# Kernel tuning notes

Measured on AMD Instinct MI355X. Metric: run time of the kernel, lower is better.

Reference implementation:

```python
import jax, jax.numpy as jnp
import numpy as np

B, S = 2, 2048                 # batch, prefill seq len
H, HKV, D = 32, 8, 128          # num_heads, num_kv_heads, head_size
G = H // HKV                    # queries per kv head (GQA)
BLOCK_SIZE, NUM_BLOCKS = 128, 128
SCALE = 1.0 / (D ** 0.5)
NEG_INF = -1e9


def setup_inputs() -> dict:
    key = jax.random.key(0)
    kq, kk, kv, kc = jax.random.split(key, 4)
    query = jax.random.normal(kq, (B, S, H * D), dtype=jnp.float32)
    key_t = jax.random.normal(kk, (B, S, HKV * D), dtype=jnp.float32)
    value = jax.random.normal(kv, (B, S, HKV * D), dtype=jnp.float32)
    kv_cache = jax.random.normal(kc, (2, NUM_BLOCKS, BLOCK_SIZE, HKV, D), dtype=jnp.float32)
    tok = jnp.arange(B * S)
    block_indices = (tok // BLOCK_SIZE).astype(jnp.int32)   # in [0, NUM_BLOCKS)
    block_offsets = (tok % BLOCK_SIZE).astype(jnp.int32)    # in [0, BLOCK_SIZE)
    causal = jnp.tril(jnp.ones((S, S), dtype=bool))
    attn_bias = jnp.where(causal, 0.0, NEG_INF).astype(jnp.float32)[None, None]  # [1,1,S,S]
    return {"query": query, "key": key_t, "value": value, "kv_cache": kv_cache,
            "block_indices": block_indices, "block_offsets": block_offsets,
            "attn_bias": attn_bias}


def reference(query, key, value, kv_cache, block_indices, block_offsets, attn_bias):
    # --- KV cache scatter write (VLLMKVCache insert) ---
    k_tok = key.reshape(-1, HKV, D)     # [num_tokens, HKV, D]
    v_tok = value.reshape(-1, HKV, D)
    key_cache = kv_cache[0].at[block_indices, block_offsets].set(k_tok)
    value_cache = kv_cache[1].at[block_indices, block_offsets].set(v_tok)

    # --- prefill attention (xops.prompt_attention with GQA) ---
    q = query.reshape(B, S, HKV, G, D)            # split heads into kv groups
    kh = key.reshape(B, S, HKV, D)
    vh = value.reshape(B, S, HKV, D)
    scores = jnp.einsum('bqhgd,bkhd->bhgqk', q, kh) * SCALE  # [B,HKV,G,S,S]
    scores = scores + attn_bias[:, :, None]                   # bias broadcast over h,g
    probs = jax.nn.softmax(scores, axis=-1)
    out = jnp.einsum('bhgqk,bkhd->bqhgd', probs, vh)          # [B,S,HKV,G,D]
    output = out.reshape(B, S, H * D)
    return output, key_cache, value_cache
```

## Files before the change

kernel.cpp:

```cpp
#include <hip/hip_runtime.h>
#include <hip/hip_bf16.h>
#include <stdint.h>

#define B_ 2
#define S_ 2048
#define HKV_ 8
#define D_ 128

#define KVB 32
#define KTILE_SH 4096
#define VTILE_SH 4096
#define LDSBUF 16384
#define NCOPY 512
#define PLANE4 4194304
#define NSLOT 16384

typedef __attribute__((ext_vector_type(8))) short bf16x8;
typedef __attribute__((ext_vector_type(16))) float f32x16;
typedef __attribute__((ext_vector_type(4))) int int4v;

typedef const __attribute__((address_space(1))) void gv_t;
typedef __attribute__((address_space(3))) void lv_t;

__device__ __forceinline__ unsigned pk2(float lo, float hi) {
  unsigned r;
  asm("v_cvt_pk_bf16_f32 %0, %1, %2" : "=v"(r) : "v"(lo), "v"(hi));
  return r;
}
__device__ __forceinline__ void plswap(unsigned& a, unsigned& b) {
  asm volatile("v_permlane32_swap_b32 %0, %1" : "+v"(a), "+v"(b));
}
__device__ __forceinline__ bf16x8 frag4(unsigned a, unsigned b, unsigned c, unsigned d) {
  union { int4v i; bf16x8 v; } u;
  u.i = int4v{(int)a, (int)b, (int)c, (int)d};
  return u.v;
}


__global__ __launch_bounds__(256)
void prep_kernel(const float* __restrict__ K, const float* __restrict__ V,
                 const int* __restrict__ bi, const int* __restrict__ bo,
                 float* __restrict__ kc, float* __restrict__ vc,
                 short* __restrict__ kimg, short* __restrict__ vimg,
                 unsigned char* __restrict__ map) {
  __shared__ float Vf[KVB * 132];
  const int bid = blockIdx.x;
  const int hg  = bid & 15;
  const int kt  = bid >> 4;
  const int kvh = hg & 7;
  const int b   = hg >> 3;
  const int tid = threadIdx.x;
  const int kv0 = kt * KVB;
  const float* kb = K + (int64_t)b * S_ * 1024 + kvh * 128;
  const float* vb = V + (int64_t)b * S_ * 1024 + kvh * 128;
  short* kimg_t = kimg + (int64_t)(hg * 64 + kt) * KTILE_SH;
  short* vimg_t = vimg + (int64_t)(hg * 64 + kt) * VTILE_SH;
#pragma unroll
  for (int i = 0; i < 4; ++i) {
    int idx = i * 256 + tid;
    int key = idx >> 5;
    int d0  = (idx & 31) * 4;
    int64_t roff = (int64_t)(kv0 + key) * 1024 + d0;
    float4 kf = *(const float4*)(kb + roff);
    float4 vf = *(const float4*)(vb + roff);
    int tok = b * S_ + kv0 + key;
    int slot = bi[tok] * 128 + bo[tok];
    *(float4*)(kc + (int64_t)slot * 1024 + kvh * 128 + d0) = kf;
    *(float4*)(vc + (int64_t)slot * 1024 + kvh * 128 + d0) = vf;
    if (d0 == 0 && kvh == 0) map[slot] = 1;
    unsigned k01 = pk2(kf.x, kf.y), k23 = pk2(kf.z, kf.w);
    int koff = (d0 >> 3) * 256 + key * 8 + (d0 & 7);
    int2 st; st.x = (int)k01; st.y = (int)k23;
    *(int2*)(kimg_t + koff) = st;
    *(float4*)(&Vf[key * 132 + d0]) = vf;
  }
  __syncthreads();
  const int d  = tid & 127;
  const int kg = tid >> 7;
  const int k0 = kg * 16;
  unsigned uu[8];
#pragma unroll
  for (int i2 = 0; i2 < 8; ++i2)
    uu[i2] = pk2(Vf[(k0 + 2 * i2) * 132 + d], Vf[(k0 + 2 * i2 + 1) * 132 + d]);
  int vbase = ((d >> 5) * 4 + (k0 >> 4) * 2) * 256 + (d & 31) * 8;
  *(int4v*)(vimg_t + vbase)       = int4v{(int)uu[0], (int)uu[1], (int)uu[2], (int)uu[3]};
  *(int4v*)(vimg_t + vbase + 256) = int4v{(int)uu[4], (int)uu[5], (int)uu[6], (int)uu[7]};
}


__global__ __launch_bounds__(256, 4)
void fused_kernel(const float* __restrict__ Q, const short* __restrict__ kimg,
                  const short* __restrict__ vimg, const float4* __restrict__ kvc,
                  float4* __restrict__ cdst, const unsigned char* __restrict__ map,
                  float* __restrict__ O) {
  __shared__ int4v ldsv[2 * LDSBUF / 16];
  char* ldsb = (char*)ldsv;

  const int bid = blockIdx.x;
  const int tid = threadIdx.x;

  if (bid < NCOPY) {
    const int n4 = 2 * PLANE4;
    for (int idx = bid * 256 + tid; idx < n4; idx += NCOPY * 256) {
      int f = idx & (PLANE4 - 1);
      if (!map[f >> 8]) cdst[idx] = kvc[idx];
    }
    return;
  }

  const int abid = bid - NCOPY;
  const int hg  = abid & 15;
  const int cc  = 63 - (abid >> 4);
  const int kvh = hg & 7;
  const int b   = hg >> 3;

  const int w   = tid >> 6;
  const int l   = tid & 63;
  const int c31 = l & 31;
  const int hi  = l >> 5;
  const int qi  = c31 & 15;
  const int hh  = c31 >> 4;
  const int qoff = cc * 32 + (w & 1) * 16;
  const int qrow = qoff + qi;
  const int h    = kvh * 4 + (w >> 1) * 2 + hh;

  const float qscale = 0.08838834764831845f * 1.4426950408889634f;

  const float* qp = Q + ((int64_t)(b * S_ + qrow)) * 4096 + h * 128;
  bf16x8 qf[8];
#pragma unroll
  for (int ks = 0; ks < 8; ++ks) {
    int d0 = ks * 16 + hi * 8;
    float4 x = *(const float4*)(qp + d0);
    float4 y = *(const float4*)(qp + d0 + 4);
    qf[ks] = frag4(pk2(x.x * qscale, x.y * qscale), pk2(x.z * qscale, x.w * qscale),
                   pk2(y.x * qscale, y.y * qscale), pk2(y.z * qscale, y.w * qscale));
  }

  f32x16 acc[4];
#pragma unroll
  for (int dt = 0; dt < 4; ++dt)
#pragma unroll
    for (int r = 0; r < 16; ++r) acc[dt][r] = 0.f;
  float m = -1e30f, lsum = 0.f;

  const int nkt = cc + 1;
  const short* kimg_b = kimg + (int64_t)(hg * 64) * KTILE_SH;
  const short* vimg_b = vimg + (int64_t)(hg * 64) * VTILE_SH;

#define STAGE(KT, BUF)                                                           \
  do {                                                                           \
    const short* kg_ = kimg_b + (int64_t)(KT) * KTILE_SH;                        \
    const short* vg_ = vimg_b + (int64_t)(KT) * VTILE_SH;                        \
    char* kd_ = ldsb + (BUF) * LDSBUF;                                           \
    char* vd_ = kd_ + 8192;                                                      \
    _Pragma("unroll")                                                            \
    for (int i_ = 0; i_ < 2; ++i_) {                                             \
      int u_ = i_ * 256 + w * 64;                                                \
      __builtin_amdgcn_global_load_lds((gv_t*)(const void*)(kg_ + (u_ + l) * 8), \
                                       (lv_t*)(void*)(kd_ + u_ * 16), 16, 0, 0); \
      __builtin_amdgcn_global_load_lds((gv_t*)(const void*)(vg_ + (u_ + l) * 8), \
                                       (lv_t*)(void*)(vd_ + u_ * 16), 16, 0, 0); \
    }                                                                            \
  } while (0)

  STAGE(0, 0);

  for (int kt = 0; kt < nkt; ++kt) {
    __syncthreads();
    const int cur = kt & 1;
    if (kt + 1 < nkt) STAGE(kt + 1, cur ^ 1);
    const char* kfr = ldsb + cur * LDSBUF + hi * 512 + c31 * 16;
    const char* vfr = kfr + 8192;
    const int kv0 = kt * KVB;

    f32x16 s;
#pragma unroll
    for (int r = 0; r < 16; ++r) s[r] = 0.f;
#pragma unroll
    for (int ks = 0; ks < 8; ++ks) {
      bf16x8 kf = *(const bf16x8*)(kfr + ks * 1024);
      s = __builtin_amdgcn_mfma_f32_32x32x16_bf16(kf, qf[ks], s, 0, 0, 0);
    }

    if (kv0 + 31 > qoff) {
#pragma unroll
      for (int r = 0; r < 16; ++r) {
        int key = kv0 + (r & 3) + 8 * (r >> 2) + 4 * hi;
        if (key > qrow) s[r] = -1e30f;
      }
    }

    float qm = fmaxf(fmaxf(s[0], s[1]), s[2]);
    qm = fmaxf(fmaxf(qm, s[3]), s[4]);
    qm = fmaxf(fmaxf(qm, s[5]), s[6]);
    qm = fmaxf(fmaxf(qm, s[7]), s[8]);
    qm = fmaxf(fmaxf(qm, s[9]), s[10]);
    qm = fmaxf(fmaxf(qm, s[11]), s[12]);
    qm = fmaxf(fmaxf(qm, s[13]), s[14]);
    qm = fmaxf(qm, s[15]);
    qm = fmaxf(qm, __shfl_xor(qm, 32));
    if (__any(qm > m + 11.0f)) {
      float mn = fmaxf(m, qm);
      float al = exp2f(m - mn);
      m = mn; lsum *= al;
#pragma unroll
      for (int dt = 0; dt < 4; ++dt)
#pragma unroll
        for (int r = 0; r < 16; ++r) acc[dt][r] *= al;
    }
    float su = 0.f;
#pragma unroll
    for (int r = 0; r < 16; ++r) {
      float p = exp2f(s[r] - m);
      s[r] = p;
      su += p;
    }
    lsum += su;

    unsigned u0 = pk2(s[0], s[1]),   u1 = pk2(s[2], s[3]);
    unsigned u2 = pk2(s[4], s[5]),   u3 = pk2(s[6], s[7]);
    unsigned u4 = pk2(s[8], s[9]),   u5 = pk2(s[10], s[11]);
    unsigned u6 = pk2(s[12], s[13]), u7 = pk2(s[14], s[15]);
    plswap(u0, u2); plswap(u1, u3);
    plswap(u4, u6); plswap(u5, u7);
    bf16x8 pf0 = frag4(u0, u1, u2, u3);
    bf16x8 pf1 = frag4(u4, u5, u6, u7);

#pragma unroll
    for (int ks2 = 0; ks2 < 2; ++ks2) {
      bf16x8 pf = ks2 ? pf1 : pf0;
#pragma unroll
      for (int dt = 0; dt < 4; ++dt) {
        bf16x8 vf = *(const bf16x8*)(vfr + (dt * 2 + ks2) * 1024);
        acc[dt] = __builtin_amdgcn_mfma_f32_32x32x16_bf16(vf, pf, acc[dt], 0, 0, 0);
      }
    }
  }
#undef STAGE

  float lt = lsum + __shfl_xor(lsum, 32);
  float inv = 1.0f / lt;
  __syncthreads();
  float* scr = (float*)ldsb + w * (32 * 33);
  float* ob = O + (int64_t)(b * S_) * 4096;
#pragma unroll
  for (int dt = 0; dt < 4; ++dt) {
#pragma unroll
    for (int r = 0; r < 16; ++r) {
      int crow = (r & 3) + 8 * (r >> 2) + 4 * hi;
      scr[c31 * 33 + crow] = acc[dt][r] * inv;
    }
    asm volatile("" ::: "memory");
#pragma unroll
    for (int rr = 0; rr < 16; ++rr) {
      int col = rr * 2 + hi;
      float val = scr[col * 33 + c31];
      int qi2 = col & 15, hh2 = col >> 4;
      int qq = cc * 32 + (w & 1) * 16 + qi2;
      int h2 = kvh * 4 + (w >> 1) * 2 + hh2;
      ob[(int64_t)qq * 4096 + h2 * 128 + dt * 32 + c31] = val;
    }
    asm volatile("" ::: "memory");
  }
}

extern "C" void kernel_launch(void* const* d_in, const int* in_sizes, int n_in,
                              void* d_out, int out_size, void* d_ws, size_t ws_size,
                              hipStream_t stream) {
  const float* Q   = (const float*)d_in[0];
  const float* K   = (const float*)d_in[1];
  const float* V   = (const float*)d_in[2];
  const float* kvc = (const float*)d_in[3];
  const int*   bi  = (const int*)d_in[4];
  const int*   bo  = (const int*)d_in[5];

  float* out = (float*)d_out;
  float* kc = out + (int64_t)B_ * S_ * 32 * 128;
  float* vc = kc + (int64_t)128 * 128 * HKV_ * D_;

  short* kimg = (short*)d_ws;
  short* vimg = kimg + (int64_t)1024 * KTILE_SH;
  unsigned char* map = (unsigned char*)(vimg + (int64_t)1024 * VTILE_SH);

  hipMemsetAsync(map, 0, NSLOT, stream);
  hipLaunchKernelGGL(prep_kernel, dim3(1024), dim3(256), 0, stream,
                     K, V, bi, bo, kc, vc, kimg, vimg, map);
  hipLaunchKernelGGL(fused_kernel, dim3(NCOPY + 1024), dim3(256), 0, stream,
                     Q, kimg, vimg, (const float4*)kvc, (float4*)kc, map, out);
}
```

Before: 194.8 us.

## Replace map-guarded cache copy with full copy plus trailing scatter kernel

Result: slower. 365.9 us (+87.8%).

```diff
diff --git a/kernel.cpp b/kernel.cpp
--- a/kernel.cpp
+++ b/kernel.cpp
@@ -11,9 +11,9 @@
 #define KTILE_SH 4096
 #define VTILE_SH 4096
 #define LDSBUF 16384
-#define NCOPY 512
+#define NATTN 1024
+#define NCOPYB 2048
 #define PLANE4 4194304
-#define NSLOT 16384
 
 typedef __attribute__((ext_vector_type(8))) short bf16x8;
 typedef __attribute__((ext_vector_type(16))) float f32x16;
@@ -39,10 +39,7 @@
 
 __global__ __launch_bounds__(256)
 void prep_kernel(const float* __restrict__ K, const float* __restrict__ V,
-                 const int* __restrict__ bi, const int* __restrict__ bo,
-                 float* __restrict__ kc, float* __restrict__ vc,
-                 short* __restrict__ kimg, short* __restrict__ vimg,
-                 unsigned char* __restrict__ map) {
+                 short* __restrict__ kimg, short* __restrict__ vimg) {
   __shared__ float Vf[KVB * 132];
   const int bid = blockIdx.x;
   const int hg  = bid & 15;
@@ -63,11 +60,6 @@
     int64_t roff = (int64_t)(kv0 + key) * 1024 + d0;
     float4 kf = *(const float4*)(kb + roff);
     float4 vf = *(const float4*)(vb + roff);
-    int tok = b * S_ + kv0 + key;
-    int slot = bi[tok] * 128 + bo[tok];
-    *(float4*)(kc + (int64_t)slot * 1024 + kvh * 128 + d0) = kf;
-    *(float4*)(vc + (int64_t)slot * 1024 + kvh * 128 + d0) = vf;
-    if (d0 == 0 && kvh == 0) map[slot] = 1;
     unsigned k01 = pk2(kf.x, kf.y), k23 = pk2(kf.z, kf.w);
     int koff = (d0 >> 3) * 256 + key * 8 + (d0 & 7);
     int2 st; st.x = (int)k01; st.y = (int)k23;
@@ -88,29 +80,40 @@
 }
 
 
+__global__ __launch_bounds__(256)
+void scatter_kernel(const float4* __restrict__ key, const float4* __restrict__ val,
+                    const int* __restrict__ bi, const int* __restrict__ bo,
+                    float4* __restrict__ kc, float4* __restrict__ vc) {
+  int idx = blockIdx.x * 256 + threadIdx.x;
+  int t = idx >> 8;
+  int rem = idx & 255;
+  int64_t slot = (int64_t)bi[t] * 128 + bo[t];
+  kc[slot * 256 + rem] = key[(int64_t)t * 256 + rem];
+  vc[slot * 256 + rem] = val[(int64_t)t * 256 + rem];
+}
+
+
 __global__ __launch_bounds__(256, 4)
 void fused_kernel(const float* __restrict__ Q, const short* __restrict__ kimg,
                   const short* __restrict__ vimg, const float4* __restrict__ kvc,
-                  float4* __restrict__ cdst, const unsigned char* __restrict__ map,
-                  float* __restrict__ O) {
+                  float4* __restrict__ cdst, float* __restrict__ O) {
   __shared__ int4v ldsv[2 * LDSBUF / 16];
   char* ldsb = (char*)ldsv;
 
   const int bid = blockIdx.x;
   const int tid = threadIdx.x;
 
-  if (bid < NCOPY) {
-    const int n4 = 2 * PLANE4;
-    for (int idx = bid * 256 + tid; idx < n4; idx += NCOPY * 256) {
-      int f = idx & (PLANE4 - 1);
-      if (!map[f >> 8]) cdst[idx] = kvc[idx];
-    }
+  if (bid >= NATTN) {
+    const int64_t base = (int64_t)(bid - NATTN) * 4096;
+    const float4* src = kvc + base;
+    float4* dst = cdst + base;
+#pragma unroll
+    for (int i = 0; i < 16; ++i) dst[i * 256 + tid] = src[i * 256 + tid];
     return;
   }
 
-  const int abid = bid - NCOPY;
-  const int hg  = abid & 15;
-  const int cc  = 63 - (abid >> 4);
+  const int hg  = bid & 15;
+  const int cc  = 63 - (bid >> 4);
   const int kvh = hg & 7;
   const int b   = hg >> 3;
 
@@ -177,11 +180,17 @@
     f32x16 s;
 #pragma unroll
     for (int r = 0; r < 16; ++r) s[r] = 0.f;
+    __builtin_amdgcn_s_setprio(1);
 #pragma unroll
     for (int ks = 0; ks < 8; ++ks) {
       bf16x8 kf = *(const bf16x8*)(kfr + ks * 1024);
       s = __builtin_amdgcn_mfma_f32_32x32x16_bf16(kf, qf[ks], s, 0, 0, 0);
     }
+    __builtin_amdgcn_s_setprio(0);
+
+    bf16x8 vfrag[8];
+#pragma unroll
+    for (int i = 0; i < 8; ++i) vfrag[i] = *(const bf16x8*)(vfr + i * 1024);
 
     if (kv0 + 31 > qoff) {
 #pragma unroll
@@ -191,14 +200,12 @@
       }
     }
 
-    float qm = fmaxf(fmaxf(s[0], s[1]), s[2]);
-    qm = fmaxf(fmaxf(qm, s[3]), s[4]);
-    qm = fmaxf(fmaxf(qm, s[5]), s[6]);
-    qm = fmaxf(fmaxf(qm, s[7]), s[8]);
-    qm = fmaxf(fmaxf(qm, s[9]), s[10]);
-    qm = fmaxf(fmaxf(qm, s[11]), s[12]);
-    qm = fmaxf(fmaxf(qm, s[13]), s[14]);
-    qm = fmaxf(qm, s[15]);
+    float a0 = fmaxf(s[0], s[1]),   a1 = fmaxf(s[2], s[3]);
+    float a2 = fmaxf(s[4], s[5]),   a3 = fmaxf(s[6], s[7]);
+    float a4 = fmaxf(s[8], s[9]),   a5 = fmaxf(s[10], s[11]);
+    float a6 = fmaxf(s[12], s[13]), a7 = fmaxf(s[14], s[15]);
+    a0 = fmaxf(a0, a1); a2 = fmaxf(a2, a3); a4 = fmaxf(a4, a5); a6 = fmaxf(a6, a7);
+    float qm = fmaxf(fmaxf(a0, a2), fmaxf(a4, a6));
     qm = fmaxf(qm, __shfl_xor(qm, 32));
     if (__any(qm > m + 11.0f)) {
       float mn = fmaxf(m, qm);
@@ -209,33 +216,34 @@
 #pragma unroll
         for (int r = 0; r < 16; ++r) acc[dt][r] *= al;
     }
-    float su = 0.f;
-#pragma unroll
-    for (int r = 0; r < 16; ++r) {
-      float p = exp2f(s[r] - m);
-      s[r] = p;
-      su += p;
-    }
-    lsum += su;
-
-    unsigned u0 = pk2(s[0], s[1]),   u1 = pk2(s[2], s[3]);
-    unsigned u2 = pk2(s[4], s[5]),   u3 = pk2(s[6], s[7]);
-    unsigned u4 = pk2(s[8], s[9]),   u5 = pk2(s[10], s[11]);
-    unsigned u6 = pk2(s[12], s[13]), u7 = pk2(s[14], s[15]);
+    float p[16];
+#pragma unroll
+    for (int r = 0; r < 16; ++r) p[r] = exp2f(s[r] - m);
+    float b0 = (p[0] + p[1]) + (p[2] + p[3]);
+    float b1 = (p[4] + p[5]) + (p[6] + p[7]);
+    float b2 = (p[8] + p[9]) + (p[10] + p[11]);
+    float b3 = (p[12] + p[13]) + (p[14] + p[15]);
+    lsum += (b0 + b1) + (b2 + b3);
+
+    unsigned u0 = pk2(p[0], p[1]),   u1 = pk2(p[2], p[3]);
+    unsigned u2 = pk2(p[4], p[5]),   u3 = pk2(p[6], p[7]);
+    unsigned u4 = pk2(p[8], p[9]),   u5 = pk2(p[10], p[11]);
+    unsigned u6 = pk2(p[12], p[13]), u7 = pk2(p[14], p[15]);
     plswap(u0, u2); plswap(u1, u3);
     plswap(u4, u6); plswap(u5, u7);
     bf16x8 pf0 = frag4(u0, u1, u2, u3);
     bf16x8 pf1 = frag4(u4, u5, u6, u7);
 
+    __builtin_amdgcn_s_setprio(1);
 #pragma unroll
     for (int ks2 = 0; ks2 < 2; ++ks2) {
       bf16x8 pf = ks2 ? pf1 : pf0;
 #pragma unroll
-      for (int dt = 0; dt < 4; ++dt) {
-        bf16x8 vf = *(const bf16x8*)(vfr + (dt * 2 + ks2) * 1024);
-        acc[dt] = __builtin_amdgcn_mfma_f32_32x32x16_bf16(vf, pf, acc[dt], 0, 0, 0);
-      }
-    }
+      for (int dt = 0; dt < 4; ++dt)
+        acc[dt] = __builtin_amdgcn_mfma_f32_32x32x16_bf16(vfrag[dt * 2 + ks2], pf,
+                                                          acc[dt], 0, 0, 0);
+    }
+    __builtin_amdgcn_s_setprio(0);
   }
 #undef STAGE
 
@@ -281,11 +289,11 @@
 
   short* kimg = (short*)d_ws;
   short* vimg = kimg + (int64_t)1024 * KTILE_SH;
-  unsigned char* map = (unsigned char*)(vimg + (int64_t)1024 * VTILE_SH);
-
-  hipMemsetAsync(map, 0, NSLOT, stream);
-  hipLaunchKernelGGL(prep_kernel, dim3(1024), dim3(256), 0, stream,
-                     K, V, bi, bo, kc, vc, kimg, vimg, map);
-  hipLaunchKernelGGL(fused_kernel, dim3(NCOPY + 1024), dim3(256), 0, stream,
-                     Q, kimg, vimg, (const float4*)kvc, (float4*)kc, map, out);
-}
+
+  hipLaunchKernelGGL(prep_kernel, dim3(1024), dim3(256), 0, stream, K, V, kimg, vimg);
+  hipLaunchKernelGGL(fused_kernel, dim3(NATTN + NCOPYB), dim3(256), 0, stream,
+                     Q, kimg, vimg, (const float4*)kvc, (float4*)kc, out);
+  hipLaunchKernelGGL(scatter_kernel, dim3(4096), dim3(256), 0, stream,
+                     (const float4*)K, (const float4*)V, bi, bo,
+                     (float4*)kc, (float4*)vc);
+}
```
